# Performance work log

Hardware: AMD Instinct MI355X
Metric: run time of the kernel (lower is better)

The kernel has to match this reference:

```python
import jax, jax.numpy as jnp
import numpy as np

N_ENVS = 8192
H = W = 64
VIEW = 11
R = VIEW // 2
EMPTY, WALL, FOOD, POISON = 0.0, 1.0, 2.0, 3.0
FOOD_REWARD = 10.0
POISON_PENALTY = 10.0
MOVE_COST = 1.0


def setup_inputs() -> dict:
    key = jax.random.key(0)
    ks = jax.random.split(key, 7)
    grids = jax.random.randint(ks[0], (N_ENVS, H, W), 0, 4).astype(jnp.float32)
    agent_energy = jax.random.uniform(ks[1], (N_ENVS,), minval=1.0, maxval=100.0, dtype=jnp.float32)
    interestingness_lut = jax.random.uniform(ks[2], (5,), dtype=jnp.float32)
    agent_x = jax.random.randint(ks[3], (N_ENVS,), 0, W).astype(jnp.int32)
    agent_y = jax.random.randint(ks[4], (N_ENVS,), 0, H).astype(jnp.int32)
    agent_steps = jax.random.randint(ks[5], (N_ENVS,), 0, 500).astype(jnp.int32)
    actions = jax.random.randint(ks[6], (N_ENVS,), 0, 9).astype(jnp.int32)
    # 3x3 neighborhood moves (dy, dx), matching MAX_MOVE_DISTANCE=1 action space
    action_deltas = jnp.array([[dy, dx] for dy in (-1, 0, 1) for dx in (-1, 0, 1)], dtype=jnp.int32)
    return dict(grids=grids, agent_energy=agent_energy, interestingness_lut=interestingness_lut,
                agent_x=agent_x, agent_y=agent_y, agent_steps=agent_steps,
                actions=actions, action_deltas=action_deltas)


def reference(grids, agent_energy, interestingness_lut, agent_x, agent_y,
              agent_steps, actions, action_deltas):
    n = grids.shape[0]
    env = jnp.arange(n)
    d = action_deltas[actions]                       # (N, 2) = (dy, dx)
    ny = jnp.clip(agent_y + d[:, 0], 0, H - 1)
    nx = jnp.clip(agent_x + d[:, 1], 0, W - 1)
    # block moves into walls: stay in place
    tgt = grids[env, ny, nx]
    blocked = tgt == WALL
    ny = jnp.where(blocked, agent_y, ny)
    nx = jnp.where(blocked, agent_x, nx)
    cell = grids[env, ny, nx]                        # cell agent lands on
    is_food = cell == FOOD
    is_poison = cell == POISON
    reward = jnp.where(is_food, FOOD_REWARD, 0.0) - jnp.where(is_poison, POISON_PENALTY, 0.0)
    consumed = is_food | is_poison
    # scatter: consumed food/poison becomes empty
    new_grids = grids.at[env, ny, nx].set(jnp.where(consumed, EMPTY, cell))
    energy = agent_energy - MOVE_COST + reward
    # local observation windows: pad with WALL, gather (VIEW, VIEW) around agent
    padded = jnp.pad(new_grids, ((0, 0), (R, R), (R, R)), constant_values=WALL)
    win = jax.vmap(lambda g, y, x: jax.lax.dynamic_slice(g, (y, x), (VIEW, VIEW)))(padded, ny, nx)  # (N, V, V)
    f32 = jnp.float32
    obs = jnp.stack([
        (win == FOOD).astype(f32),
        (win == POISON).astype(f32),
        (win == WALL).astype(f32),
        interestingness_lut[win.astype(jnp.int32)],
        win,
        jnp.broadcast_to(energy[:, None, None], (n, VIEW, VIEW)),
    ], axis=1)                                       # (N, 6, V, V)
    return obs
```

## Files before the change

### kernel.cpp

```cpp
#include <hip/hip_runtime.h>

#define NVIEW 11
#define RAD 5
#define GH 64
#define GW 64
#define WINSZ (NVIEW * NVIEW)
#define NCH 6
#define NOUT (NCH * WINSZ)

__global__ __launch_bounds__(128) void env_step_obs_kernel(
    const float* __restrict__ grids,
    const float* __restrict__ agent_energy,
    const float* __restrict__ lut,
    const int*   __restrict__ agent_x,
    const int*   __restrict__ agent_y,
    const int*   __restrict__ actions,
    const int*   __restrict__ action_deltas,
    float*       __restrict__ out)
{
    const int n   = blockIdx.x;
    const int tid = threadIdx.x;

    __shared__ float s_win[WINSZ];
    __shared__ float s_lut[5];
    __shared__ float s_energy;

    const int a  = actions[n];
    const int dy = action_deltas[2 * a];
    const int dx = action_deltas[2 * a + 1];
    const int y0 = agent_y[n];
    const int x0 = agent_x[n];

    int ny = min(max(y0 + dy, 0), GH - 1);
    int nx = min(max(x0 + dx, 0), GW - 1);

    const float* g = grids + (size_t)n * (GH * GW);

    const float tgt = g[ny * GW + nx];
    if (tgt == 1.0f) { ny = y0; nx = x0; }

    const float cell      = g[ny * GW + nx];
    const bool  is_food   = (cell == 2.0f);
    const bool  is_poison = (cell == 3.0f);
    const bool  consumed  = is_food || is_poison;
    const float reward    = (is_food ? 10.0f : 0.0f) - (is_poison ? 10.0f : 0.0f);

    if (tid < 5)  s_lut[tid] = lut[tid];
    if (tid == 0) s_energy   = agent_energy[n] - 1.0f + reward;

    if (tid < WINSZ) {
        const int i  = tid / NVIEW;
        const int j  = tid - i * NVIEW;
        const int yy = ny - RAD + i;
        const int xx = nx - RAD + j;
        float v;
        if (yy < 0 || yy >= GH || xx < 0 || xx >= GW) {
            v = 1.0f;
        } else {
            v = g[yy * GW + xx];
        }
        if (consumed && tid == (RAD * NVIEW + RAD)) v = 0.0f;
        s_win[tid] = v;
    }
    __syncthreads();

    const float energy = s_energy;
    float* o_base = out + (size_t)n * NOUT;
    #pragma unroll
    for (int o = tid; o < NOUT; o += 128) {
        const int   c = o / WINSZ;
        const int   p = o - c * WINSZ;
        const float v = s_win[p];
        float r;
        switch (c) {
            case 0:  r = (v == 2.0f) ? 1.0f : 0.0f; break;
            case 1:  r = (v == 3.0f) ? 1.0f : 0.0f; break;
            case 2:  r = (v == 1.0f) ? 1.0f : 0.0f; break;
            case 3:  r = s_lut[(int)v];             break;
            case 4:  r = v;                         break;
            default: r = energy;                    break;
        }
        o_base[o] = r;
    }
}

extern "C" void kernel_launch(void* const* d_in, const int* in_sizes, int n_in,
                              void* d_out, int out_size, void* d_ws, size_t ws_size,
                              hipStream_t stream) {
    const float* grids   = (const float*)d_in[0];
    const float* energy  = (const float*)d_in[1];
    const float* lut     = (const float*)d_in[2];
    const int*   agent_x = (const int*)d_in[3];
    const int*   agent_y = (const int*)d_in[4];
    const int*   actions = (const int*)d_in[6];
    const int*   deltas  = (const int*)d_in[7];
    float*       out     = (float*)d_out;

    const int n_envs = in_sizes[1];

    env_step_obs_kernel<<<n_envs, 128, 0, stream>>>(
        grids, energy, lut, agent_x, agent_y, actions, deltas, out);
}
```

Measured before the change: 190.9 us.

## Map one wavefront per environment and drop shared memory staging

Each 64-lane wavefront now handles one environment, with four environments per 256-thread block. Every lane keeps its window cells in registers and writes all six channels directly, which removes the shared-memory staging, the block barrier and the per-element channel switch. The LUT lookup becomes a select chain over four preloaded values, which assumes grid values stay in 0..3. The second pass leaves many lanes idle because only 121 cells are spread over 128 lanes, and stores are strided across channels.

Result: no change. 188.1 us (-1.4%).

```diff
diff --git a/kernel.cpp b/kernel.cpp
--- a/kernel.cpp
+++ b/kernel.cpp
@@ -8,7 +8,7 @@
 #define NCH 6
 #define NOUT (NCH * WINSZ)
 
-__global__ __launch_bounds__(128) void env_step_obs_kernel(
+__global__ __launch_bounds__(256) void env_step_obs_kernel(
     const float* __restrict__ grids,
     const float* __restrict__ agent_energy,
     const float* __restrict__ lut,
@@ -16,14 +16,13 @@
     const int*   __restrict__ agent_y,
     const int*   __restrict__ actions,
     const int*   __restrict__ action_deltas,
-    float*       __restrict__ out)
+    float*       __restrict__ out,
+    int n_envs)
 {
-    const int n   = blockIdx.x;
-    const int tid = threadIdx.x;
-
-    __shared__ float s_win[WINSZ];
-    __shared__ float s_lut[5];
-    __shared__ float s_energy;
+    const int lane = threadIdx.x & 63;
+    const int wave = threadIdx.x >> 6;
+    const int n    = blockIdx.x * 4 + wave;
+    if (n >= n_envs) return;
 
     const int a  = actions[n];
     const int dy = action_deltas[2 * a];
@@ -44,43 +43,42 @@
     const bool  is_poison = (cell == 3.0f);
     const bool  consumed  = is_food || is_poison;
     const float reward    = (is_food ? 10.0f : 0.0f) - (is_poison ? 10.0f : 0.0f);
+    const float energy    = agent_energy[n] - 1.0f + reward;
 
-    if (tid < 5)  s_lut[tid] = lut[tid];
-    if (tid == 0) s_energy   = agent_energy[n] - 1.0f + reward;
+    const float l0 = lut[0], l1 = lut[1], l2 = lut[2], l3 = lut[3];
 
-    if (tid < WINSZ) {
-        const int i  = tid / NVIEW;
-        const int j  = tid - i * NVIEW;
-        const int yy = ny - RAD + i;
-        const int xx = nx - RAD + j;
-        float v;
-        if (yy < 0 || yy >= GH || xx < 0 || xx >= GW) {
-            v = 1.0f;
-        } else {
-            v = g[yy * GW + xx];
+    float v[2];
+    #pragma unroll
+    for (int r = 0; r < 2; ++r) {
+        const int p = lane + r * 64;
+        float val = 1.0f;
+        if (p < WINSZ) {
+            const int i  = p / NVIEW;
+            const int j  = p - i * NVIEW;
+            const int yy = ny - RAD + i;
+            const int xx = nx - RAD + j;
+            if (yy >= 0 && yy < GH && xx >= 0 && xx < GW) val = g[yy * GW + xx];
+            if (consumed && p == (RAD * NVIEW + RAD)) val = 0.0f;
         }
-        if (consumed && tid == (RAD * NVIEW + RAD)) v = 0.0f;
-        s_win[tid] = v;
+        v[r] = val;
     }
-    __syncthreads();
 
-    const float energy = s_energy;
-    float* o_base = out + (size_t)n * NOUT;
+    float* ob = out + (size_t)n * NOUT;
     #pragma unroll
-    for (int o = tid; o < NOUT; o += 128) {
-        const int   c = o / WINSZ;
-        const int   p = o - c * WINSZ;
-        const float v = s_win[p];
-        float r;
-        switch (c) {
-            case 0:  r = (v == 2.0f) ? 1.0f : 0.0f; break;
-            case 1:  r = (v == 3.0f) ? 1.0f : 0.0f; break;
-            case 2:  r = (v == 1.0f) ? 1.0f : 0.0f; break;
-            case 3:  r = s_lut[(int)v];             break;
-            case 4:  r = v;                         break;
-            default: r = energy;                    break;
+    for (int r = 0; r < 2; ++r) {
+        const int p = lane + r * 64;
+        if (p < WINSZ) {
+            const float val = v[r];
+            ob[0 * WINSZ + p] = (val == 2.0f) ? 1.0f : 0.0f;
+            ob[1 * WINSZ + p] = (val == 3.0f) ? 1.0f : 0.0f;
+            ob[2 * WINSZ + p] = (val == 1.0f) ? 1.0f : 0.0f;
+            const float lv = (val == 0.0f) ? l0
+                           : (val == 1.0f) ? l1
+                           : (val == 2.0f) ? l2 : l3;
+            ob[3 * WINSZ + p] = lv;
+            ob[4 * WINSZ + p] = val;
+            ob[5 * WINSZ + p] = energy;
         }
-        o_base[o] = r;
     }
 }
 
@@ -97,7 +95,8 @@
     float*       out     = (float*)d_out;
 
     const int n_envs = in_sizes[1];
+    const int blocks = (n_envs + 3) / 4;
 
-    env_step_obs_kernel<<<n_envs, 128, 0, stream>>>(
-        grids, energy, lut, agent_x, agent_y, actions, deltas, out);
+    env_step_obs_kernel<<<blocks, 256, 0, stream>>>(
+        grids, energy, lut, agent_x, agent_y, actions, deltas, out, n_envs);
 }
```
